# Performance work log

Measured on AMD Instinct MI355X. Metric: run time of the kernel, lower is better.

The kernel has to match this reference:

```python
import jax, jax.numpy as jnp
import numpy as np

# Mamba2 config derived from __init__ defaults
D_MODEL, D_STATE, D_CONV, EXPAND, HEADDIM = 768, 16, 4, 2, 64
D_INNER = EXPAND * D_MODEL                      # 1536
NHEADS = D_INNER // HEADDIM                     # 24
NGROUPS = 1
CONV_DIM = D_INNER + 2 * NGROUPS * D_STATE      # 1568
D_IN_PROJ = 2 * D_INNER + 2 * NGROUPS * D_STATE + NHEADS  # 3128
EPS = 1e-5


def setup_inputs() -> dict:
    key = jax.random.key(0)
    ks = jax.random.split(key, 8)
    B, L = 2, 4096
    x = jax.random.normal(ks[0], (B, L, D_MODEL), jnp.float32)
    s_in = 1.0 / np.sqrt(D_MODEL)
    s_out = 1.0 / np.sqrt(D_INNER)
    W_in = jax.random.uniform(ks[1], (D_IN_PROJ, D_MODEL), jnp.float32, -s_in, s_in)
    W_out = jax.random.uniform(ks[2], (D_MODEL, D_INNER), jnp.float32, -s_out, s_out)
    conv_w = jax.random.uniform(ks[3], (CONV_DIM, D_CONV), jnp.float32, -0.5, 0.5)
    conv_b = jax.random.uniform(ks[4], (CONV_DIM,), jnp.float32, -0.5, 0.5)
    # dt init in [1e-3, 0.1] (log-uniform), stored as inverse-softplus bias
    dt = jnp.exp(jax.random.uniform(ks[5], (NHEADS,), jnp.float32) * (np.log(0.1) - np.log(1e-3)) + np.log(1e-3))
    dt_bias = dt + jnp.log(-jnp.expm1(-dt))
    A_log = jnp.log(jax.random.uniform(ks[6], (NHEADS,), jnp.float32, 1.0, 16.0))
    D = jnp.ones((NHEADS,), jnp.float32)
    ln_w = jnp.ones((D_MODEL,), jnp.float32)
    ln_b = jnp.zeros((D_MODEL,), jnp.float32)
    gate_norm_w = jnp.ones((D_INNER,), jnp.float32)
    return dict(x=x, ln_w=ln_w, ln_b=ln_b, W_in=W_in, conv_w=conv_w, conv_b=conv_b,
                dt_bias=dt_bias, A_log=A_log, D=D, gate_norm_w=gate_norm_w, W_out=W_out)


def _layernorm(x, w, b):
    mu = x.mean(-1, keepdims=True)
    var = ((x - mu) ** 2).mean(-1, keepdims=True)
    return (x - mu) * jax.lax.rsqrt(var + EPS) * w + b


def _silu(x):
    return x * jax.nn.sigmoid(x)


def _mamba_block(x, ln_w, ln_b, W_in, conv_w, conv_b, dt_bias, A_log, D, gate_norm_w, W_out):
    Bsz, L, _ = x.shape
    u = _layernorm(x, ln_w, ln_b)
    zxbcdt = jnp.einsum('bld,ed->ble', u, W_in)                 # (b,l,3128)
    z = zxbcdt[..., :D_INNER]
    xBC = zxbcdt[..., D_INNER:D_INNER + CONV_DIM]
    dt = jax.nn.softplus(zxbcdt[..., -NHEADS:] + dt_bias)       # (b,l,h)
    # causal depthwise conv (width D_CONV) + SiLU
    xp = jnp.pad(xBC, ((0, 0), (D_CONV - 1, 0), (0, 0)))
    acc = xp[:, 0:L, :] * conv_w[:, 0]
    for i in range(1, D_CONV):
        acc = acc + xp[:, i:i + L, :] * conv_w[:, i]
    xBC = _silu(acc + conv_b)
    xs = xBC[..., :D_INNER].reshape(Bsz, L, NHEADS, HEADDIM)    # (b,l,h,p)
    Bm = xBC[..., D_INNER:D_INNER + D_STATE]                    # (b,l,n) ngroups=1
    Cm = xBC[..., D_INNER + D_STATE:]                           # (b,l,n)
    A = -jnp.exp(A_log)                                         # (h,)
    dA = jnp.exp(dt * A)                                        # (b,l,h)
    # selective scan: h_t = dA_t * h_{t-1} + dt_t * (x_t outer B_t)
    def step(h, inp):
        dA_t, dt_t, B_t, C_t, x_t = inp                          # (b,h),(b,h),(b,n),(b,n),(b,h,p)
        h = dA_t[..., None, None] * h + jnp.einsum('bh,bn,bhp->bhpn', dt_t, B_t, x_t)
        y = jnp.einsum('bhpn,bn->bhp', h, C_t)
        return h, y
    h0 = jnp.zeros((Bsz, NHEADS, HEADDIM, D_STATE), x.dtype)
    _, ys = jax.lax.scan(step, h0, (dA.transpose(1, 0, 2), dt.transpose(1, 0, 2),
                                    Bm.transpose(1, 0, 2), Cm.transpose(1, 0, 2),
                                    xs.transpose(1, 0, 2, 3)))
    y = ys.transpose(1, 0, 2, 3) + D[:, None] * xs               # (b,l,h,p) skip term
    y = y.reshape(Bsz, L, D_INNER)
    # gated RMSNorm: norm(y * silu(z)) * weight
    g = y * _silu(z)
    g = g * jax.lax.rsqrt((g * g).mean(-1, keepdims=True) + EPS) * gate_norm_w
    out = jnp.einsum('ble,de->bld', g, W_out)
    return x + out


def reference(x, ln_w, ln_b, W_in, conv_w, conv_b, dt_bias, A_log, D, gate_norm_w, W_out):
    return _mamba_block(x, ln_w, ln_b, W_in, conv_w, conv_b, dt_bias, A_log, D, gate_norm_w, W_out)
```

## Files before the change

### kernel.cpp

```cpp
#include <hip/hip_runtime.h>
#include <hip/hip_bf16.h>
#include <stdint.h>

#define SEQ      4096
#define BATCH    2
#define NTOK     (BATCH*SEQ)
#define DMODEL   768
#define DINNER   1536
#define NHEADS   24
#define HEADDIM  64
#define DSTATE   16
#define NPAD     3200
#define EPSV     1e-5f
#define CHUNK    64
#define NCHUNK   (SEQ/CHUNK)
#define SUB      32
#define LNBLK    2048

typedef __bf16 bf16x8 __attribute__((ext_vector_type(8)));
typedef float  floatx4 __attribute__((ext_vector_type(4)));

__device__ __forceinline__ unsigned short f2bf(float f) {
    union { float f; uint32_t u; } v; v.f = f;
    uint32_t u = v.u;
    uint32_t r = (u + 0x7fffu + ((u >> 16) & 1u)) >> 16;
    return (unsigned short)r;
}

__device__ __forceinline__ float bf2f(unsigned short h) {
    union { uint32_t u; float f; } v; v.u = (uint32_t)h << 16;
    return v.f;
}

__device__ __forceinline__ float bfl(uint32_t u) {
    union { uint32_t u; float f; } v; v.u = u << 16; return v.f;
}
__device__ __forceinline__ float bfh(uint32_t u) {
    union { uint32_t u; float f; } v; v.u = u & 0xffff0000u; return v.f;
}

__device__ __forceinline__ float siluf(float x) { return x / (1.f + __expf(-x)); }

__device__ __forceinline__ void async_cp16(const void* g, void* l) {
    __builtin_amdgcn_global_load_lds(
        (const __attribute__((address_space(1))) void*)g,
        (__attribute__((address_space(3))) void*)l,
        16, 0, 0);
}

__global__ __launch_bounds__(256) void prep_kernel(
    const float* __restrict__ x, const float* __restrict__ lnw, const float* __restrict__ lnb,
    unsigned short* __restrict__ u16,
    const float* __restrict__ Win, const float* __restrict__ Wout,
    const float* __restrict__ gw,
    unsigned short* __restrict__ win16, unsigned short* __restrict__ wout16)
{
    if (blockIdx.x < LNBLK) {
        int wave = threadIdx.x >> 6, lane = threadIdx.x & 63;
        int token = blockIdx.x * 4 + wave;
        const float* row = x + (size_t)token * DMODEL;
        float4 v[3];
        float s = 0.f, ss = 0.f;
#pragma unroll
        for (int j = 0; j < 3; ++j) {
            v[j] = *(const float4*)(row + lane*4 + j*256);
            s  += v[j].x + v[j].y + v[j].z + v[j].w;
            ss += v[j].x*v[j].x + v[j].y*v[j].y + v[j].z*v[j].z + v[j].w*v[j].w;
        }
#pragma unroll
        for (int o = 32; o > 0; o >>= 1) { s += __shfl_xor(s, o, 64); ss += __shfl_xor(ss, o, 64); }
        float mean = s * (1.f/768.f);
        float var  = ss * (1.f/768.f) - mean*mean;
        float rstd = rsqrtf(var + EPSV);
        unsigned short* brow = u16 + (size_t)token * DMODEL;
#pragma unroll
        for (int j = 0; j < 3; ++j) {
            int cidx = lane*4 + j*256;
            float4 w4 = *(const float4*)(lnw + cidx);
            float4 b4 = *(const float4*)(lnb + cidx);
            float a0 = (v[j].x - mean)*rstd*w4.x + b4.x;
            float a1 = (v[j].y - mean)*rstd*w4.y + b4.y;
            float a2 = (v[j].z - mean)*rstd*w4.z + b4.z;
            float a3 = (v[j].w - mean)*rstd*w4.w + b4.w;
            ushort4 p; p.x = f2bf(a0); p.y = f2bf(a1); p.z = f2bf(a2); p.w = f2bf(a3);
            *(ushort4*)(brow + cidx) = p;
        }
    } else {
        int e = ((blockIdx.x - LNBLK) * 256 + threadIdx.x) * 4;
        const int n1 = NPAD * DMODEL;
        if (e < n1) {
            int r = e / DMODEL;
            ushort4 p = {0, 0, 0, 0};
            if (r < 3128) {
                float4 v = *(const float4*)(Win + e);
                p.x = f2bf(v.x); p.y = f2bf(v.y); p.z = f2bf(v.z); p.w = f2bf(v.w);
            }
            *(ushort4*)(win16 + e) = p;
        } else {
            int e2 = e - n1;
            if (e2 < DMODEL * DINNER) {
                int row = e2 / DINNER;
                int col = e2 - row * DINNER;
                float4 v = *(const float4*)(Wout + e2);
                float4 w = *(const float4*)(gw + col);
                ushort4 p; p.x = f2bf(v.x*w.x); p.y = f2bf(v.y*w.y);
                           p.z = f2bf(v.z*w.z); p.w = f2bf(v.w*w.w);
                *(ushort4*)(wout16 + e2) = p;
            }
        }
    }
}

__global__ __launch_bounds__(256, 3) void gemm1_kernel(
    const unsigned short* __restrict__ A, const unsigned short* __restrict__ Bt,
    unsigned short* __restrict__ z16, unsigned short* __restrict__ x16,
    float* __restrict__ bcr, float* __restrict__ raw24)
{
    constexpr int K = DMODEL;
    __shared__ unsigned short As[128*64];
    __shared__ unsigned short Bs[128*64];
    const int tid  = threadIdx.x;
    const int lane = tid & 63;
    const int wave = tid >> 6;
    const int id   = blockIdx.x;
    const int xcd  = id & 7;
    const int j5   = id >> 3;
    const int m0 = (xcd*8 + (j5 & 7)) * 128;
    const int n0 = (j5 >> 3) * 128;
    const int wm = (wave & 1) * 64;
    const int wn = (wave >> 1) * 64;

    floatx4 acc[4][4];
#pragma unroll
    for (int i = 0; i < 4; ++i)
#pragma unroll
        for (int j = 0; j < 4; ++j) acc[i][j] = floatx4{0.f, 0.f, 0.f, 0.f};

    const int srow8  = lane >> 3;
    const int schunk = lane & 7;
    const int sscol  = (schunk ^ srow8) * 8;

    for (int k0 = 0; k0 < K; k0 += 64) {
        __syncthreads();
#pragma unroll
        for (int o = 0; o < 4; ++o) {
            int row = wave*32 + o*8 + srow8;
            async_cp16(A + (size_t)(m0 + row) * K + k0 + sscol, As + row*64 + schunk*8);
        }
#pragma unroll
        for (int o = 0; o < 4; ++o) {
            int row = wave*32 + o*8 + srow8;
            async_cp16(Bt + (size_t)(n0 + row) * K + k0 + sscol, Bs + row*64 + schunk*8);
        }
        __syncthreads();
        const int fr  = lane & 15;
        const int q8  = lane >> 4;
        const int key = fr & 7;
#pragma unroll
        for (int ks = 0; ks < 2; ++ks) {
            const int ch = ((ks*4 + q8) ^ key) * 8;
            bf16x8 a[4], b[4];
#pragma unroll
            for (int i = 0; i < 4; ++i)
                a[i] = *(const bf16x8*)(As + (wm + i*16 + fr)*64 + ch);
#pragma unroll
            for (int j = 0; j < 4; ++j)
                b[j] = *(const bf16x8*)(Bs + (wn + j*16 + fr)*64 + ch);
#pragma unroll
            for (int i = 0; i < 4; ++i)
#pragma unroll
                for (int j = 0; j < 4; ++j)
                    acc[i][j] = __builtin_amdgcn_mfma_f32_16x16x32_bf16(a[i], b[j], acc[i][j], 0, 0, 0);
        }
    }

    const int col = lane & 15;
    const int rq  = (lane >> 4) * 4;
    if (n0 < DINNER) {
#pragma unroll
        for (int i = 0; i < 4; ++i)
#pragma unroll
            for (int j = 0; j < 4; ++j)
#pragma unroll
                for (int r = 0; r < 4; ++r) {
                    int gm = m0 + wm + i*16 + rq + r;
                    int gn = n0 + wn + j*16 + col;
                    z16[(size_t)gm * DINNER + gn] = f2bf(acc[i][j][r]);
                }
    } else if (n0 < 3072) {
#pragma unroll
        for (int i = 0; i < 4; ++i)
#pragma unroll
            for (int j = 0; j < 4; ++j)
#pragma unroll
                for (int r = 0; r < 4; ++r) {
                    int gm = m0 + wm + i*16 + rq + r;
                    int gn = n0 + wn + j*16 + col;
                    x16[(size_t)gm * DINNER + (gn - DINNER)] = f2bf(acc[i][j][r]);
                }
    } else {
#pragma unroll
        for (int i = 0; i < 4; ++i)
#pragma unroll
            for (int j = 0; j < 4; ++j)
#pragma unroll
                for (int r = 0; r < 4; ++r) {
                    int gm = m0 + wm + i*16 + rq + r;
                    int gn = n0 + wn + j*16 + col;
                    if (gn < 3104)
                        bcr[(size_t)gm * 32 + (gn - 3072)] = acc[i][j][r];
                    else if (gn < 3128)
                        raw24[(size_t)gm * NHEADS + (gn - 3104)] = acc[i][j][r];
                }
    }
}

__global__ __launch_bounds__(256, 3) void gemm2_kernel(
    const unsigned short* __restrict__ A, const unsigned short* __restrict__ Bt,
    float* __restrict__ Cf, const float* __restrict__ resid)
{
    constexpr int K = DINNER;
    __shared__ unsigned short As[2][64*64];
    __shared__ unsigned short Bs[2][128*64];
    __shared__ float rowss[64];
    const int tid  = threadIdx.x;
    const int lane = tid & 63;
    const int wave = tid >> 6;
    const int id   = blockIdx.x;
    const int xcd  = id & 7;
    const int j6   = id >> 3;
    const int m0 = (xcd*16 + j6/6) * 64;
    const int n0 = (j6 % 6) * 128;
    const int wm = (wave & 1) * 32;
    const int wn = (wave >> 1) * 64;

    floatx4 acc[2][4];
#pragma unroll
    for (int i = 0; i < 2; ++i)
#pragma unroll
        for (int j = 0; j < 4; ++j) acc[i][j] = floatx4{0.f, 0.f, 0.f, 0.f};

    const int srow8  = lane >> 3;
    const int schunk = lane & 7;
    const int sscol  = (schunk ^ srow8) * 8;

    const int sr0 = tid >> 3;
    const int scc = ((tid & 7) ^ (sr0 & 7)) * 8;
    float rs0 = 0.f, rs1 = 0.f;

    for (int k0 = 0; k0 < K; k0 += 128) {
        __syncthreads();
#pragma unroll
        for (int hh = 0; hh < 2; ++hh) {
#pragma unroll
            for (int o = 0; o < 2; ++o) {
                int row = wave*16 + o*8 + srow8;
                async_cp16(A + (size_t)(m0 + row) * K + k0 + hh*64 + sscol,
                           &As[hh][row*64 + schunk*8]);
            }
#pragma unroll
            for (int o = 0; o < 4; ++o) {
                int row = wave*32 + o*8 + srow8;
                async_cp16(Bt + (size_t)(n0 + row) * K + k0 + hh*64 + sscol,
                           &Bs[hh][row*64 + schunk*8]);
            }
        }
        __syncthreads();
        const int fr  = lane & 15;
        const int q8  = lane >> 4;
        const int key = fr & 7;
#pragma unroll
        for (int hh = 0; hh < 2; ++hh) {
#pragma unroll
            for (int ks = 0; ks < 2; ++ks) {
                const int ch = ((ks*4 + q8) ^ key) * 8;
                bf16x8 a[2], b[4];
#pragma unroll
                for (int i = 0; i < 2; ++i)
                    a[i] = *(const bf16x8*)(&As[hh][(wm + i*16 + fr)*64 + ch]);
#pragma unroll
                for (int j = 0; j < 4; ++j)
                    b[j] = *(const bf16x8*)(&Bs[hh][(wn + j*16 + fr)*64 + ch]);
#pragma unroll
                for (int i = 0; i < 2; ++i)
#pragma unroll
                    for (int j = 0; j < 4; ++j)
                        acc[i][j] = __builtin_amdgcn_mfma_f32_16x16x32_bf16(a[i], b[j], acc[i][j], 0, 0, 0);
            }
            bf16x8 q0 = *(const bf16x8*)(&As[hh][sr0*64 + scc]);
            bf16x8 q1 = *(const bf16x8*)(&As[hh][(sr0 + 32)*64 + scc]);
#pragma unroll
            for (int e = 0; e < 8; ++e) {
                float f0 = (float)q0[e]; rs0 += f0*f0;
                float f1 = (float)q1[e]; rs1 += f1*f1;
            }
        }
    }

    rs0 += __shfl_xor(rs0, 1, 64); rs0 += __shfl_xor(rs0, 2, 64); rs0 += __shfl_xor(rs0, 4, 64);
    rs1 += __shfl_xor(rs1, 1, 64); rs1 += __shfl_xor(rs1, 2, 64); rs1 += __shfl_xor(rs1, 4, 64);
    if ((lane & 7) == 0) {
        rowss[wave*8 + (lane >> 3)]      = rs0;
        rowss[wave*8 + 32 + (lane >> 3)] = rs1;
    }
    __syncthreads();

    const int col = lane & 15;
    const int rq  = (lane >> 4) * 4;
#pragma unroll
    for (int i = 0; i < 2; ++i)
#pragma unroll
        for (int r = 0; r < 4; ++r) {
            int lrow = wm + i*16 + rq + r;
            int gm = m0 + lrow;
            float sc = rsqrtf(rowss[lrow] * (1.f/1536.f) + EPSV);
#pragma unroll
            for (int j = 0; j < 4; ++j) {
                int gn = n0 + wn + j*16 + col;
                Cf[(size_t)gm * DMODEL + gn] = acc[i][j][r] * sc + resid[(size_t)gm * DMODEL + gn];
            }
        }
}

__global__ __launch_bounds__(256) void scan_pass1(
    const unsigned short* __restrict__ x16, const float* __restrict__ bcr,
    const float* __restrict__ raw24, const float* __restrict__ dt_bias,
    const float* __restrict__ A_log,
    const float* __restrict__ cw, const float* __restrict__ cb, const float* __restrict__ Dp,
    float* __restrict__ hloc, float* __restrict__ pprod,
    unsigned short* __restrict__ ylocal16, float* __restrict__ dAT)
{
    int wave = threadIdx.x >> 6, lane = threadIdx.x & 63;
    int blk = blockIdx.x * 4 + wave;
    int c = blk & (NCHUNK-1), bh = blk >> 6;
    int h = bh % NHEADS, b = bh / NHEADS;
    int row0 = b * SEQ + c * CHUNK;
    int l0 = c * CHUNK;
    int tb = h * NTOK + row0;
    __shared__ float bcraw[4][35][32];
    __shared__ float bcsc[4][32][32];
    __shared__ float av[4][32], dv[4][32];

    const int cx = h*64 + lane;
    float cwx0 = cw[cx*4+0], cwx1 = cw[cx*4+1], cwx2 = cw[cx*4+2], cwx3 = cw[cx*4+3];
    float cbx = cb[cx];
    const int nBC = lane & 31;
    float cwc0 = cw[(DINNER+nBC)*4+0], cwc1 = cw[(DINNER+nBC)*4+1];
    float cwc2 = cw[(DINNER+nBC)*4+2], cwc3 = cw[(DINNER+nBC)*4+3];
    float cbc = cb[DINNER+nBC];
    float Dh = Dp[h];
    float dtb = dt_bias[h];
    float Ah  = -__expf(A_log[h]);

    float xm3 = (l0 >= 3) ? bf2f(x16[(size_t)(row0-3)*DINNER + cx]) : 0.f;
    float xm2 = (l0 >= 2) ? bf2f(x16[(size_t)(row0-2)*DINNER + cx]) : 0.f;
    float xm1 = (l0 >= 1) ? bf2f(x16[(size_t)(row0-1)*DINNER + cx]) : 0.f;

    float hst[16];
#pragma unroll
    for (int n = 0; n < 16; ++n) hst[n] = 0.f;
    float aprod = 1.f;

    for (int sc = 0; sc < CHUNK/SUB; ++sc) {
        int rb = row0 + sc * SUB;
        int lb = l0 + sc * SUB;
        __syncthreads();
#pragma unroll
        for (int it = 0; it < 5; ++it) {
            int idx = it*64 + lane;
            if (idx < 280) {
                int s = idx >> 3, q = idx & 7;
                float4 val = {0.f,0.f,0.f,0.f};
                if (lb - 3 + s >= 0)
                    val = *(const float4*)(bcr + (size_t)(rb-3+s)*32 + q*4);
                *(float4*)&bcraw[wave][s][q*4] = val;
            }
        }
        if (lane < 32) {
            float raw = raw24[(size_t)(rb + lane)*NHEADS + h] + dtb;
            float dt = (raw > 20.f) ? raw : log1pf(__expf(raw));
            float dA = __expf(dt * Ah);
            av[wave][lane] = dA;
            dv[wave][lane] = dt;
            dAT[(size_t)tb + sc*SUB + lane] = dA;
        }
        float xr[SUB];
#pragma unroll
        for (int s = 0; s < SUB; ++s)
            xr[s] = bf2f(x16[(size_t)(rb+s)*DINNER + cx]);
        __syncthreads();
#pragma unroll
        for (int it = 0; it < 16; ++it) {
            int s = it*2 + (lane >> 5);
            float v = cbc + bcraw[wave][s][nBC]*cwc0 + bcraw[wave][s+1][nBC]*cwc1
                          + bcraw[wave][s+2][nBC]*cwc2 + bcraw[wave][s+3][nBC]*cwc3;
            bcsc[wave][s][nBC] = siluf(v);
        }
        __syncthreads();
#pragma unroll 2
        for (int s = 0; s < SUB; ++s) {
            float a = av[wave][s];
            float xc = siluf(cbx + xm3*cwx0 + xm2*cwx1 + xm1*cwx2 + xr[s]*cwx3);
            xm3 = xm2; xm2 = xm1; xm1 = xr[s];
            float scale = dv[wave][s] * xc;
            float y = Dh * xc;
            const float4* bp4 = (const float4*)&bcsc[wave][s][0];
            float4 bv[8];
#pragma unroll
            for (int q = 0; q < 8; ++q) bv[q] = bp4[q];
            const float* bp = (const float*)bv;
#pragma unroll
            for (int n = 0; n < 16; ++n) hst[n] = a*hst[n] + scale*bp[n];
#pragma unroll
            for (int n = 0; n < 16; ++n) y += hst[n] * bp[16+n];
            aprod *= a;
            ylocal16[(size_t)(rb+s)*DINNER + cx] = f2bf(y);
        }
    }
    float* o = hloc + (size_t)blk * 1024 + lane * 16;
#pragma unroll
    for (int n = 0; n < 16; ++n) o[n] = hst[n];
    if (lane == 0) pprod[blk] = aprod;
}

__global__ __launch_bounds__(256) void scan_pass2(
    const float* __restrict__ hloc, const float* __restrict__ pprod, float* __restrict__ hstart)
{
    __shared__ float sm[64*256];
    __shared__ float pp[64];
    const int tid = threadIdx.x;
    const int bh  = blockIdx.x >> 2;
    const int q   = blockIdx.x & 3;
    const float* src = hloc + (size_t)bh * 65536 + q * 256;
#pragma unroll
    for (int it = 0; it < 16; ++it) {
        int idx = it*256 + tid;
        int c   = idx >> 6;
        int e4  = (idx & 63) * 4;
        *(float4*)&sm[c*256 + e4] = *(const float4*)(src + (size_t)c*1024 + e4);
    }
    if (tid < 64) pp[tid] = pprod[bh*64 + tid];
    __syncthreads();
    float h = 0.f;
    float* dst = hstart + (size_t)bh * 65536 + q * 256 + tid;
#pragma unroll 8
    for (int c = 0; c < 64; ++c) {
        dst[(size_t)c * 1024] = h;
        h = pp[c] * h + sm[c*256 + tid];
    }
}

__global__ __launch_bounds__(256) void scan_pass3(
    const float* __restrict__ bcr, const float* __restrict__ dAT,
    const float* __restrict__ cw, const float* __restrict__ cb,
    const float* __restrict__ hstart, const unsigned short* __restrict__ z16,
    unsigned short* __restrict__ ylocal16)
{
    int wave = threadIdx.x >> 6, lane = threadIdx.x & 63;
    int blk = blockIdx.x * 4 + wave;
    int c = blk & (NCHUNK-1), bh = blk >> 6;
    int h = bh % NHEADS, b = bh / NHEADS;
    int row0 = b * SEQ + c * CHUNK;
    int l0 = c * CHUNK;
    int tb = h * NTOK + row0;
    __shared__ float craw[4][35][16];
    __shared__ float csc[4][32][16];
    __shared__ float av[4][32];

    const int cx = h*64 + lane;
    const int nC = lane & 15;
    float cwc0 = cw[(DINNER+16+nC)*4+0], cwc1 = cw[(DINNER+16+nC)*4+1];
    float cwc2 = cw[(DINNER+16+nC)*4+2], cwc3 = cw[(DINNER+16+nC)*4+3];
    float cbc = cb[DINNER+16+nC];

    float h0[16];
    const float* hs = hstart + (size_t)blk * 1024 + lane * 16;
#pragma unroll
    for (int n = 0; n < 16; ++n) h0[n] = hs[n];
    float cd = 1.f;

    for (int sc = 0; sc < CHUNK/SUB; ++sc) {
        int rb = row0 + sc * SUB;
        int lb = l0 + sc * SUB;
        __syncthreads();
#pragma unroll
        for (int it = 0; it < 3; ++it) {
            int idx = it*64 + lane;
            if (idx < 140) {
                int s = idx >> 2, q = idx & 3;
                float4 val = {0.f,0.f,0.f,0.f};
                if (lb - 3 + s >= 0)
                    val = *(const float4*)(bcr + (size_t)(rb-3+s)*32 + 16 + q*4);
                *(float4*)&craw[wave][s][q*4] = val;
            }
        }
        if (lane < 32) av[wave][lane] = dAT[(size_t)tb + sc*SUB + lane];
        float yr[SUB], zr[SUB];
#pragma unroll
        for (int s = 0; s < SUB; ++s) {
            yr[s] = bf2f(ylocal16[(size_t)(rb+s)*DINNER + cx]);
            zr[s] = bf2f(z16[(size_t)(rb+s)*DINNER + cx]);
        }
        __syncthreads();
#pragma unroll
        for (int it = 0; it < 8; ++it) {
            int s = it*4 + (lane >> 4);
            float v = cbc + craw[wave][s][nC]*cwc0 + craw[wave][s+1][nC]*cwc1
                          + craw[wave][s+2][nC]*cwc2 + craw[wave][s+3][nC]*cwc3;
            csc[wave][s][nC] = siluf(v);
        }
        __syncthreads();
#pragma unroll 2
        for (int s = 0; s < SUB; ++s) {
            cd *= av[wave][s];
            const float4* cp4 = (const float4*)&csc[wave][s][0];
            float4 cv[4];
#pragma unroll
            for (int q = 0; q < 4; ++q) cv[q] = cp4[q];
            const float* cp = (const float*)cv;
            float corr = 0.f;
#pragma unroll
            for (int n = 0; n < 16; ++n) corr += cp[n] * h0[n];
            float g = (yr[s] + cd * corr) * siluf(zr[s]);
            ylocal16[(size_t)(rb+s)*DINNER + cx] = f2bf(g);
        }
    }
}

extern "C" void kernel_launch(void* const* d_in, const int* in_sizes, int n_in,
                              void* d_out, int out_size, void* d_ws, size_t ws_size,
                              hipStream_t stream)
{
    const float* x        = (const float*)d_in[0];
    const float* ln_w     = (const float*)d_in[1];
    const float* ln_b     = (const float*)d_in[2];
    const float* W_in     = (const float*)d_in[3];
    const float* conv_w   = (const float*)d_in[4];
    const float* conv_b   = (const float*)d_in[5];
    const float* dt_bias  = (const float*)d_in[6];
    const float* A_log    = (const float*)d_in[7];
    const float* Dp       = (const float*)d_in[8];
    const float* gate_w   = (const float*)d_in[9];
    const float* W_out    = (const float*)d_in[10];
    float* out = (float*)d_out;

    char* ws = (char*)d_ws;
    size_t off = 0;
    auto alloc = [&](size_t bytes) -> void* {
        void* p = ws + off;
        off += (bytes + 255) & ~(size_t)255;
        return p;
    };
    unsigned short* u16    = (unsigned short*)alloc((size_t)NTOK*DMODEL*2);
    unsigned short* win16  = (unsigned short*)alloc((size_t)NPAD*DMODEL*2);
    float*          dAT    = (float*)alloc((size_t)NTOK*NHEADS*4);
    float*          raw24  = (float*)alloc((size_t)NTOK*NHEADS*4);
    unsigned short* x16    = (unsigned short*)alloc((size_t)NTOK*DINNER*2);
    float*          bcr    = (float*)alloc((size_t)NTOK*32*4);
    unsigned short* wout16 = (unsigned short*)alloc((size_t)DMODEL*DINNER*2);
    unsigned short* z16    = (unsigned short*)alloc((size_t)NTOK*DINNER*2);
    unsigned short* y16    = (unsigned short*)alloc((size_t)NTOK*DINNER*2);
    unsigned short* g16    = (unsigned short*)alloc((size_t)NTOK*DINNER*2);
    float*          pprod  = (float*)alloc((size_t)BATCH*NHEADS*NCHUNK*4);
    float* hloc   = (float*)u16;
    float* hstart = (float*)g16;

    prep_kernel<<<LNBLK + (NPAD*DMODEL + DMODEL*DINNER)/1024, 256, 0, stream>>>(
        x, ln_w, ln_b, u16, W_in, W_out, gate_w, win16, wout16);
    gemm1_kernel<<<1600, 256, 0, stream>>>(u16, win16, z16, x16, bcr, raw24);
    scan_pass1<<<BATCH*NHEADS*NCHUNK/4, 256, 0, stream>>>(
        x16, bcr, raw24, dt_bias, A_log, conv_w, conv_b, Dp, hloc, pprod, y16, dAT);
    scan_pass2<<<BATCH*NHEADS*4, 256, 0, stream>>>(hloc, pprod, hstart);
    scan_pass3<<<BATCH*NHEADS*NCHUNK/4, 256, 0, stream>>>(bcr, dAT, conv_w, conv_b, hstart, z16, y16);
    gemm2_kernel<<<768, 256, 0, stream>>>(y16, wout16, out, x);
}
```

Measured before the change: 257.2 us.

## Restructure chunked scan: pass1 computes states only, pass3 reruns scan from carried-in state

Pass 1 now only runs the B-side recurrence to produce per-chunk end states and decay products, without computing C projections or writing the intermediate y to global memory. Pass 3 starts from the true carried-in state and reruns the full recurrence to produce y, applying the skip term and SiLU gate directly. This removes the bf16 intermediate y write and re-read plus the separate correction term. In exchange the recurrence is computed twice and a dt buffer is added. The output also avoids the rounding of y through bf16 before the correction.

```diff
diff --git a/kernel.cpp b/kernel.cpp
--- a/kernel.cpp
+++ b/kernel.cpp
@@ -326,9 +326,132 @@
     const unsigned short* __restrict__ x16, const float* __restrict__ bcr,
     const float* __restrict__ raw24, const float* __restrict__ dt_bias,
     const float* __restrict__ A_log,
+    const float* __restrict__ cw, const float* __restrict__ cb,
+    float* __restrict__ hloc, float* __restrict__ pprod,
+    float* __restrict__ dAT, float* __restrict__ dtT)
+{
+    int wave = threadIdx.x >> 6, lane = threadIdx.x & 63;
+    int blk = blockIdx.x * 4 + wave;
+    int c = blk & (NCHUNK-1), bh = blk >> 6;
+    int h = bh % NHEADS, b = bh / NHEADS;
+    int row0 = b * SEQ + c * CHUNK;
+    int l0 = c * CHUNK;
+    int tb = h * NTOK + row0;
+    __shared__ float braw[4][35][16];
+    __shared__ float bsc[4][32][16];
+    __shared__ float av[4][32], dv[4][32];
+
+    const int cx = h*64 + lane;
+    float cwx0 = cw[cx*4+0], cwx1 = cw[cx*4+1], cwx2 = cw[cx*4+2], cwx3 = cw[cx*4+3];
+    float cbx = cb[cx];
+    const int nB = lane & 15;
+    float cwb0 = cw[(DINNER+nB)*4+0], cwb1 = cw[(DINNER+nB)*4+1];
+    float cwb2 = cw[(DINNER+nB)*4+2], cwb3 = cw[(DINNER+nB)*4+3];
+    float cbb = cb[DINNER+nB];
+    float dtb = dt_bias[h];
+    float Ah  = -__expf(A_log[h]);
+
+    float xm3 = (l0 >= 3) ? bf2f(x16[(size_t)(row0-3)*DINNER + cx]) : 0.f;
+    float xm2 = (l0 >= 2) ? bf2f(x16[(size_t)(row0-2)*DINNER + cx]) : 0.f;
+    float xm1 = (l0 >= 1) ? bf2f(x16[(size_t)(row0-1)*DINNER + cx]) : 0.f;
+
+    float hst[16];
+#pragma unroll
+    for (int n = 0; n < 16; ++n) hst[n] = 0.f;
+    float aprod = 1.f;
+
+    for (int sc = 0; sc < CHUNK/SUB; ++sc) {
+        int rb = row0 + sc * SUB;
+        int lb = l0 + sc * SUB;
+        __syncthreads();
+#pragma unroll
+        for (int it = 0; it < 3; ++it) {
+            int idx = it*64 + lane;
+            if (idx < 140) {
+                int s = idx >> 2, q = idx & 3;
+                float4 val = {0.f,0.f,0.f,0.f};
+                if (lb - 3 + s >= 0)
+                    val = *(const float4*)(bcr + (size_t)(rb-3+s)*32 + q*4);
+                *(float4*)&braw[wave][s][q*4] = val;
+            }
+        }
+        if (lane < 32) {
+            float raw = raw24[(size_t)(rb + lane)*NHEADS + h] + dtb;
+            float dt = (raw > 20.f) ? raw : log1pf(__expf(raw));
+            float dA = __expf(dt * Ah);
+            av[wave][lane] = dA;
+            dv[wave][lane] = dt;
+            dAT[(size_t)tb + sc*SUB + lane] = dA;
+            dtT[(size_t)tb + sc*SUB + lane] = dt;
+        }
+        float xr[SUB];
+#pragma unroll
+        for (int s = 0; s < SUB; ++s)
+            xr[s] = bf2f(x16[(size_t)(rb+s)*DINNER + cx]);
+        __syncthreads();
+#pragma unroll
+        for (int it = 0; it < 8; ++it) {
+            int s = it*4 + (lane >> 4);
+            float v = cbb + braw[wave][s][nB]*cwb0 + braw[wave][s+1][nB]*cwb1
+                          + braw[wave][s+2][nB]*cwb2 + braw[wave][s+3][nB]*cwb3;
+            bsc[wave][s][nB] = siluf(v);
+        }
+        __syncthreads();
+#pragma unroll 2
+        for (int s = 0; s < SUB; ++s) {
+            float a = av[wave][s];
+            float xc = siluf(cbx + xm3*cwx0 + xm2*cwx1 + xm1*cwx2 + xr[s]*cwx3);
+            xm3 = xm2; xm2 = xm1; xm1 = xr[s];
+            float scale = dv[wave][s] * xc;
+            const float4* bp4 = (const float4*)&bsc[wave][s][0];
+            float4 bv[4];
+#pragma unroll
+            for (int q = 0; q < 4; ++q) bv[q] = bp4[q];
+            const float* bp = (const float*)bv;
+#pragma unroll
+            for (int n = 0; n < 16; ++n) hst[n] = a*hst[n] + scale*bp[n];
+            aprod *= a;
+        }
+    }
+    float* o = hloc + (size_t)blk * 1024 + lane * 16;
+#pragma unroll
+    for (int n = 0; n < 16; ++n) o[n] = hst[n];
+    if (lane == 0) pprod[blk] = aprod;
+}
+
+__global__ __launch_bounds__(256) void scan_pass2(
+    const float* __restrict__ hloc, const float* __restrict__ pprod, float* __restrict__ hstart)
+{
+    __shared__ float sm[64*256];
+    __shared__ float pp[64];
+    const int tid = threadIdx.x;
+    const int bh  = blockIdx.x >> 2;
+    const int q   = blockIdx.x & 3;
+    const float* src = hloc + (size_t)bh * 65536 + q * 256;
+#pragma unroll
+    for (int it = 0; it < 16; ++it) {
+        int idx = it*256 + tid;
+        int c   = idx >> 6;
+        int e4  = (idx & 63) * 4;
+        *(float4*)&sm[c*256 + e4] = *(const float4*)(src + (size_t)c*1024 + e4);
+    }
+    if (tid < 64) pp[tid] = pprod[bh*64 + tid];
+    __syncthreads();
+    float h = 0.f;
+    float* dst = hstart + (size_t)bh * 65536 + q * 256 + tid;
+#pragma unroll 8
+    for (int c = 0; c < 64; ++c) {
+        dst[(size_t)c * 1024] = h;
+        h = pp[c] * h + sm[c*256 + tid];
+    }
+}
+
+__global__ __launch_bounds__(256) void scan_pass3(
+    const unsigned short* __restrict__ x16, const float* __restrict__ bcr,
+    const float* __restrict__ dAT, const float* __restrict__ dtT,
     const float* __restrict__ cw, const float* __restrict__ cb, const float* __restrict__ Dp,
-    float* __restrict__ hloc, float* __restrict__ pprod,
-    unsigned short* __restrict__ ylocal16, float* __restrict__ dAT)
+    const float* __restrict__ hstart, const unsigned short* __restrict__ z16,
+    unsigned short* __restrict__ yout16)
 {
     int wave = threadIdx.x >> 6, lane = threadIdx.x & 63;
     int blk = blockIdx.x * 4 + wave;
@@ -349,17 +472,15 @@
     float cwc2 = cw[(DINNER+nBC)*4+2], cwc3 = cw[(DINNER+nBC)*4+3];
     float cbc = cb[DINNER+nBC];
     float Dh = Dp[h];
-    float dtb = dt_bias[h];
-    float Ah  = -__expf(A_log[h]);
 
     float xm3 = (l0 >= 3) ? bf2f(x16[(size_t)(row0-3)*DINNER + cx]) : 0.f;
     float xm2 = (l0 >= 2) ? bf2f(x16[(size_t)(row0-2)*DINNER + cx]) : 0.f;
     float xm1 = (l0 >= 1) ? bf2f(x16[(size_t)(row0-1)*DINNER + cx]) : 0.f;
 
     float hst[16];
-#pragma unroll
-    for (int n = 0; n < 16; ++n) hst[n] = 0.f;
-    float aprod = 1.f;
+    const float* hs = hstart + (size_t)blk * 1024 + lane * 16;
+#pragma unroll
+    for (int n = 0; n < 16; ++n) hst[n] = hs[n];
 
     for (int sc = 0; sc < CHUNK/SUB; ++sc) {
         int rb = row0 + sc * SUB;
@@ -376,18 +497,14 @@
                 *(float4*)&bcraw[wave][s][q*4] = val;
             }
         }
-        if (lane < 32) {
-            float raw = raw24[(size_t)(rb + lane)*NHEADS + h] + dtb;
-            float dt = (raw > 20.f) ? raw : log1pf(__expf(raw));
-            float dA = __expf(dt * Ah);
-            av[wave][lane] = dA;
-            dv[wave][lane] = dt;
-            dAT[(size_t)tb + sc*SUB + lane] = dA;
-        }
-        float xr[SUB];
-#pragma unroll
-        for (int s = 0; s < SUB; ++s)
+        if (lane < 32) av[wave][lane] = dAT[(size_t)tb + sc*SUB + lane];
+        else           dv[wave][lane-32] = dtT[(size_t)tb + sc*SUB + lane - 32];
+        float xr[SUB], zr[SUB];
+#pragma unroll
+        for (int s = 0; s < SUB; ++s) {
             xr[s] = bf2f(x16[(size_t)(rb+s)*DINNER + cx]);
+            zr[s] = bf2f(z16[(size_t)(rb+s)*DINNER + cx]);
+        }
         __syncthreads();
 #pragma unroll
         for (int it = 0; it < 16; ++it) {
@@ -413,116 +530,8 @@
             for (int n = 0; n < 16; ++n) hst[n] = a*hst[n] + scale*bp[n];
 #pragma unroll
             for (int n = 0; n < 16; ++n) y += hst[n] * bp[16+n];
-            aprod *= a;
-            ylocal16[(size_t)(rb+s)*DINNER + cx] = f2bf(y);
-        }
-    }
-    float* o = hloc + (size_t)blk * 1024 + lane * 16;
-#pragma unroll
-    for (int n = 0; n < 16; ++n) o[n] = hst[n];
-    if (lane == 0) pprod[blk] = aprod;
-}
-
-__global__ __launch_bounds__(256) void scan_pass2(
-    const float* __restrict__ hloc, const float* __restrict__ pprod, float* __restrict__ hstart)
-{
-    __shared__ float sm[64*256];
-    __shared__ float pp[64];
-    const int tid = threadIdx.x;
-    const int bh  = blockIdx.x >> 2;
-    const int q   = blockIdx.x & 3;
-    const float* src = hloc + (size_t)bh * 65536 + q * 256;
-#pragma unroll
-    for (int it = 0; it < 16; ++it) {
-        int idx = it*256 + tid;
-        int c   = idx >> 6;
-        int e4  = (idx & 63) * 4;
-        *(float4*)&sm[c*256 + e4] = *(const float4*)(src + (size_t)c*1024 + e4);
-    }
-    if (tid < 64) pp[tid] = pprod[bh*64 + tid];
-    __syncthreads();
-    float h = 0.f;
-    float* dst = hstart + (size_t)bh * 65536 + q * 256 + tid;
-#pragma unroll 8
-    for (int c = 0; c < 64; ++c) {
-        dst[(size_t)c * 1024] = h;
-        h = pp[c] * h + sm[c*256 + tid];
-    }
-}
-
-__global__ __launch_bounds__(256) void scan_pass3(
-    const float* __restrict__ bcr, const float* __restrict__ dAT,
-    const float* __restrict__ cw, const float* __restrict__ cb,
-    const float* __restrict__ hstart, const unsigned short* __restrict__ z16,
-    unsigned short* __restrict__ ylocal16)
-{
-    int wave = threadIdx.x >> 6, lane = threadIdx.x & 63;
-    int blk = blockIdx.x * 4 + wave;
-    int c = blk & (NCHUNK-1), bh = blk >> 6;
-    int h = bh % NHEADS, b = bh / NHEADS;
-    int row0 = b * SEQ + c * CHUNK;
-    int l0 = c * CHUNK;
-    int tb = h * NTOK + row0;
-    __shared__ float craw[4][35][16];
-    __shared__ float csc[4][32][16];
-    __shared__ float av[4][32];
-
-    const int cx = h*64 + lane;
-    const int nC = lane & 15;
-    float cwc0 = cw[(DINNER+16+nC)*4+0], cwc1 = cw[(DINNER+16+nC)*4+1];
-    float cwc2 = cw[(DINNER+16+nC)*4+2], cwc3 = cw[(DINNER+16+nC)*4+3];
-    float cbc = cb[DINNER+16+nC];
-
-    float h0[16];
-    const float* hs = hstart + (size_t)blk * 1024 + lane * 16;
-#pragma unroll
-    for (int n = 0; n < 16; ++n) h0[n] = hs[n];
-    float cd = 1.f;
-
-    for (int sc = 0; sc < CHUNK/SUB; ++sc) {
-        int rb = row0 + sc * SUB;
-        int lb = l0 + sc * SUB;
-        __syncthreads();
-#pragma unroll
-        for (int it = 0; it < 3; ++it) {
-            int idx = it*64 + lane;
-            if (idx < 140) {
-                int s = idx >> 2, q = idx & 3;
-                float4 val = {0.f,0.f,0.f,0.f};
-                if (lb - 3 + s >= 0)
-                    val = *(const float4*)(bcr + (size_t)(rb-3+s)*32 + 16 + q*4);
-                *(float4*)&craw[wave][s][q*4] = val;
-            }
-        }
-        if (lane < 32) av[wave][lane] = dAT[(size_t)tb + sc*SUB + lane];
-        float yr[SUB], zr[SUB];
-#pragma unroll
-        for (int s = 0; s < SUB; ++s) {
-            yr[s] = bf2f(ylocal16[(size_t)(rb+s)*DINNER + cx]);
-            zr[s] = bf2f(z16[(size_t)(rb+s)*DINNER + cx]);
-        }
-        __syncthreads();
-#pragma unroll
-        for (int it = 0; it < 8; ++it) {
-            int s = it*4 + (lane >> 4);
-            float v = cbc + craw[wave][s][nC]*cwc0 + craw[wave][s+1][nC]*cwc1
-                          + craw[wave][s+2][nC]*cwc2 + craw[wave][s+3][nC]*cwc3;
-            csc[wave][s][nC] = siluf(v);
-        }
-        __syncthreads();
-#pragma unroll 2
-        for (int s = 0; s < SUB; ++s) {
-            cd *= av[wave][s];
-            const float4* cp4 = (const float4*)&csc[wave][s][0];
-            float4 cv[4];
-#pragma unroll
-            for (int q = 0; q < 4; ++q) cv[q] = cp4[q];
-            const float* cp = (const float*)cv;
-            float corr = 0.f;
-#pragma unroll
-            for (int n = 0; n < 16; ++n) corr += cp[n] * h0[n];
-            float g = (yr[s] + cd * corr) * siluf(zr[s]);
-            ylocal16[(size_t)(rb+s)*DINNER + cx] = f2bf(g);
+            float g = y * siluf(zr[s]);
+            yout16[(size_t)(rb+s)*DINNER + cx] = f2bf(g);
         }
     }
 }
@@ -554,6 +563,7 @@
     unsigned short* u16    = (unsigned short*)alloc((size_t)NTOK*DMODEL*2);
     unsigned short* win16  = (unsigned short*)alloc((size_t)NPAD*DMODEL*2);
     float*          dAT    = (float*)alloc((size_t)NTOK*NHEADS*4);
+    float*          dtT    = (float*)alloc((size_t)NTOK*NHEADS*4);
     float*          raw24  = (float*)alloc((size_t)NTOK*NHEADS*4);
     unsigned short* x16    = (unsigned short*)alloc((size_t)NTOK*DINNER*2);
     float*          bcr    = (float*)alloc((size_t)NTOK*32*4);
@@ -569,8 +579,9 @@
         x, ln_w, ln_b, u16, W_in, W_out, gate_w, win16, wout16);
     gemm1_kernel<<<1600, 256, 0, stream>>>(u16, win16, z16, x16, bcr, raw24);
     scan_pass1<<<BATCH*NHEADS*NCHUNK/4, 256, 0, stream>>>(
-        x16, bcr, raw24, dt_bias, A_log, conv_w, conv_b, Dp, hloc, pprod, y16, dAT);
+        x16, bcr, raw24, dt_bias, A_log, conv_w, conv_b, hloc, pprod, dAT, dtT);
     scan_pass2<<<BATCH*NHEADS*4, 256, 0, stream>>>(hloc, pprod, hstart);
-    scan_pass3<<<BATCH*NHEADS*NCHUNK/4, 256, 0, stream>>>(bcr, dAT, conv_w, conv_b, hstart, z16, y16);
+    scan_pass3<<<BATCH*NHEADS*NCHUNK/4, 256, 0, stream>>>(
+        x16, bcr, dAT, dtT, conv_w, conv_b, Dp, hstart, z16, y16);
     gemm2_kernel<<<768, 256, 0, stream>>>(y16, wout16, out, x);
 }
```

Result: no change. 260.0 us (+1.1%).
